# Kernel tuning notes

Measured on AMD Instinct MI355X. Metric: run time of the kernel, lower is better.

Reference implementation:

```python
import jax, jax.numpy as jnp
import numpy as np

B, T, DIM = 4, 1024, 2048
N_HEADS, N_KV_HEADS = 32, 8
HEAD_DIM = DIM // N_HEADS  # 64
N_REPS = N_HEADS // N_KV_HEADS  # 4


def setup_inputs() -> dict:
    key = jax.random.key(0)
    ks = jax.random.split(key, 8)
    # RoPE tables: theta = 10000^{-2i/d}, positions 0..T-1
    inv_freq = 1.0 / (10000.0 ** (jnp.arange(0, HEAD_DIM, 2, dtype=jnp.float32) / HEAD_DIM))
    angles = jnp.arange(T, dtype=jnp.float32)[:, None] * inv_freq[None, :]  # (T, HEAD_DIM//2)
    s = 0.02
    return {
        "input": jax.random.normal(ks[0], (B, T, DIM), jnp.float32),
        "freqs_cos": jnp.cos(angles),
        "freqs_sin": jnp.sin(angles),
        "mask": jnp.tril(jnp.ones((T, T), dtype=bool)),  # causal boolean mask
        "wq": s * jax.random.normal(ks[1], (DIM, DIM), jnp.float32),
        "wk": s * jax.random.normal(ks[2], (N_KV_HEADS * HEAD_DIM, DIM), jnp.float32),
        "wv": s * jax.random.normal(ks[3], (N_KV_HEADS * HEAD_DIM, DIM), jnp.float32),
        "wo": s * jax.random.normal(ks[4], (DIM, DIM), jnp.float32),
        "curr_pos": 0,
    }


def _apply_rope(x, cos, sin):
    # x: (B, T, H, D); cos/sin: (T, D//2). Complex multiply on (even, odd) pairs.
    xr = x[..., 0::2]
    xi = x[..., 1::2]
    c = cos[None, :, None, :]
    s = sin[None, :, None, :]
    out_r = xr * c - xi * s
    out_i = xr * s + xi * c
    return jnp.stack([out_r, out_i], axis=-1).reshape(x.shape)


def reference(input, freqs_cos, freqs_sin, mask, wq, wk, wv, wo, curr_pos):
    Bv, Tv = input.shape[0], input.shape[1]
    qs = (input @ wq.T).reshape(Bv, Tv, N_HEADS, HEAD_DIM)
    ks = (input @ wk.T).reshape(Bv, Tv, N_KV_HEADS, HEAD_DIM)
    vs = (input @ wv.T).reshape(Bv, Tv, N_KV_HEADS, HEAD_DIM)
    qs = _apply_rope(qs, freqs_cos, freqs_sin)
    ks = _apply_rope(ks, freqs_cos, freqs_sin)

    # KV cache (prefill path: curr_pos == 0, fresh cache of length 2T)
    kv_cache = jnp.zeros((Bv, 2 * Tv, N_KV_HEADS, HEAD_DIM, 2), input.dtype)
    kv_cache = kv_cache.at[:, curr_pos:curr_pos + Tv, :, :, 0].set(ks)
    kv_cache = kv_cache.at[:, curr_pos:curr_pos + Tv, :, :, 1].set(vs)
    k_all = kv_cache[:, :curr_pos + Tv, :, :, 0]
    v_all = kv_cache[:, :curr_pos + Tv, :, :, 1]

    # GQA: broadcast each kv head across its query-head group (avoid repeat_interleave copy)
    S = k_all.shape[1]
    q = qs.transpose(0, 2, 1, 3).reshape(Bv, N_KV_HEADS, N_REPS, Tv, HEAD_DIM)
    k = k_all.transpose(0, 2, 1, 3)  # (B, KVH, S, D)
    v = v_all.transpose(0, 2, 1, 3)

    scale = 1.0 / jnp.sqrt(jnp.asarray(HEAD_DIM, input.dtype))
    scores = jnp.einsum("bgrqd,bgkd->bgrqk", q, k) * scale  # (B, KVH, REPS, T, S)
    neg = jnp.asarray(jnp.finfo(input.dtype).min, input.dtype)
    scores = jnp.where(mask[None, None, None, :, :S], scores, neg)
    attn = jax.nn.softmax(scores, axis=-1)
    out = jnp.einsum("bgrqk,bgkd->bgrqd", attn, v)
    out = out.reshape(Bv, N_HEADS, Tv, HEAD_DIM).transpose(0, 2, 1, 3).reshape(Bv, Tv, DIM)
    return out @ wo.T
```

## Files before the change

### kernel.cpp

```cpp
#include <hip/hip_runtime.h>
#include <cstdint>

typedef __bf16 bf16x8 __attribute__((ext_vector_type(8)));
typedef float  f32x4  __attribute__((ext_vector_type(4)));
typedef float  f32x16 __attribute__((ext_vector_type(16)));
typedef float  float8v __attribute__((ext_vector_type(8)));
typedef unsigned short ushort8v __attribute__((ext_vector_type(8)));
typedef unsigned short ushort4v __attribute__((ext_vector_type(4)));
typedef unsigned int   uint4v   __attribute__((ext_vector_type(4)));

__device__ __forceinline__ unsigned short f2b(float f) {
  uint32_t u = __builtin_bit_cast(uint32_t, f);
  u += 0x7FFFu + ((u >> 16) & 1u);
  return (unsigned short)(u >> 16);
}
__device__ __forceinline__ float b2f(unsigned short h) {
  uint32_t u = ((uint32_t)h) << 16;
  return __builtin_bit_cast(float, u);
}
__device__ __forceinline__ unsigned int cvtpk(float lo, float hi_) {
  unsigned int r;
  asm("v_cvt_pk_bf16_f32 %0, %1, %2" : "=v"(r) : "v"(lo), "v"(hi_));
  return r;
}

__device__ __forceinline__ void async16(const void* g, void* l) {
  __builtin_amdgcn_global_load_lds(
      (const __attribute__((address_space(1))) void*)g,
      (__attribute__((address_space(3))) void*)l, 16, 0, 0);
}

#define WAITVM(N)  __builtin_amdgcn_s_waitcnt(0x0F70 | ((N) & 15))

struct CvtArgs {
  const float* src[5];
  unsigned short* dst[5];
  long n[5];
};
__global__ void cvt5_kernel(CvtArgs a) {
  long base = (long)blockIdx.x * blockDim.x + threadIdx.x;
  long gstride = (long)gridDim.x * blockDim.x;
#pragma unroll 1
  for (int sg = 0; sg < 5; ++sg) {
    const float* s = a.src[sg];
    unsigned short* d = a.dst[sg];
    long n8 = a.n[sg] >> 3;
    for (long i = base; i < n8; i += gstride) {
      float8v f = *(const float8v*)(s + i * 8);
      ushort8v o;
#pragma unroll
      for (int j = 0; j < 8; ++j) o[j] = f2b(f[j]);
      *(ushort8v*)(d + i * 8) = o;
    }
  }
}

__global__ __launch_bounds__(512, 2)
void gemmQ192(const unsigned short* __restrict__ Ag, const unsigned short* __restrict__ Wg,
              unsigned short* __restrict__ Cp) {
  constexpr int K = 2048;
  constexpr int NF = 3;
  constexpr int ASLOT = 16384;
  constexpr int BSLOT = 24576;
  constexpr int N = 3072;

  extern __shared__ char lds_c[];

  const int tid = threadIdx.x;
  const int wave = tid >> 6, lane = tid & 63;
  const int wm = wave >> 2, wn = wave & 3;
  const int lr = lane & 15, lg = lane >> 4;

  const int flat = blockIdx.y * 16 + blockIdx.x;
  const int swz = (flat & 7) * 32 + (flat >> 3);
  const int m0 = (swz >> 4) * 256, n0 = (swz & 15) * 192;

  const int laneSw = (lr >> 1) * 128 + (((((lr & 1) << 2) | lg) ^ (lr >> 1)) << 4);
  const int aoff = wm * 8192 + laneSw;

  int bByte[NF], bR7[NF];
#pragma unroll
  for (int ni = 0; ni < NF; ++ni) {
    int row = wn * 48 + ni * 16 + lr;
    bByte[ni] = row * 128;
    bR7[ni] = row & 7;
  }

  f32x4 acc[8][NF] = {};
  bf16x8 af[4], bf[NF];

  auto stA = [&](int slot, int s) {
    char* sl = lds_c + slot * ASLOT;
    const int kc = s * 32;
#pragma unroll
    for (int j = 0; j < 2; ++j) {
      int q = (tid + 512 * j) * 16;
      int R = q >> 7, g2L = ((q >> 4) & 7) ^ (R & 7);
      int row = R * 2 + (g2L >> 2), kg = g2L & 3;
      async16(Ag + (size_t)(m0 + row) * K + kc + kg * 8, sl + q);
    }
  };
  auto stB = [&](int slot, int T) {
    char* sl = lds_c + 4 * ASLOT + slot * BSLOT;
    const int kc = T * 64;
#pragma unroll
    for (int j = 0; j < 3; ++j) {
      int q = (tid + 512 * j) * 16;
      int row = q >> 7, c = (q >> 4) & 7;
      async16(Wg + (size_t)(n0 + row) * K + kc + ((c ^ (row & 7)) * 8), sl + q);
    }
  };

#define PH(SA, SB, MH, KH, RDB, STG, VM)                                      \
  {                                                                           \
    const char* As_ = lds_c + (SA) * ASLOT;                                   \
    _Pragma("unroll") for (int mi = 0; mi < 4; ++mi)                          \
      af[mi] = *(const bf16x8*)(As_ + aoff + ((MH) * 4 + mi) * 1024);         \
    if (RDB) {                                                                \
      const char* Bs_ = lds_c + 4 * ASLOT + (SB) * BSLOT;                     \
      _Pragma("unroll") for (int ni = 0; ni < NF; ++ni)                       \
        bf[ni] = *(const bf16x8*)(Bs_ + bByte[ni] +                           \
                                  (((((KH) << 2) | lg) ^ bR7[ni]) << 4));     \
    }                                                                         \
    STG;                                                                      \
    if ((VM) >= 0) WAITVM(VM);                                                \
    __builtin_amdgcn_s_barrier();                                             \
    __builtin_amdgcn_s_setprio(1);                                            \
    _Pragma("unroll") for (int mi = 0; mi < 4; ++mi)                          \
      _Pragma("unroll") for (int ni = 0; ni < NF; ++ni)                       \
        acc[(MH) * 4 + mi][ni] = __builtin_amdgcn_mfma_f32_16x16x32_bf16(     \
            af[mi], bf[ni], acc[(MH) * 4 + mi][ni], 0, 0, 0);                 \
    __builtin_amdgcn_s_setprio(0);                                            \
    __builtin_amdgcn_s_barrier();                                             \
  }

  stB(0, 0); stA(0, 0); stA(1, 1); stB(1, 1); stA(2, 2);
  WAITVM(5);
  __builtin_amdgcn_s_barrier();

  for (int t2 = 0; t2 < 30; t2 += 2) {
    PH(0, 0, 0, 0, true,  stA(3, 2 * t2 + 3), -1);
    PH(0, 0, 1, 0, false, (void)0, -1);
    PH(1, 0, 0, 1, true,  stA(0, 2 * t2 + 4), -1);
    PH(1, 0, 1, 1, false, stB(0, t2 + 2), 5);
    PH(2, 1, 0, 0, true,  stA(1, 2 * t2 + 5), -1);
    PH(2, 1, 1, 0, false, (void)0, -1);
    PH(3, 1, 0, 1, true,  stA(2, 2 * t2 + 6), -1);
    PH(3, 1, 1, 1, false, stB(1, t2 + 3), 5);
  }
  PH(0, 0, 0, 0, true,  stA(3, 63), -1);
  PH(0, 0, 1, 0, false, (void)0, -1);
  PH(1, 0, 0, 1, true,  (void)0, -1);
  PH(1, 0, 1, 1, false, (void)0, 0);
  PH(2, 1, 0, 0, true,  (void)0, -1);
  PH(2, 1, 1, 0, false, (void)0, -1);
  PH(3, 1, 0, 1, true,  (void)0, -1);
  PH(3, 1, 1, 1, false, (void)0, -1);
#undef PH

#pragma unroll
  for (int mig = 0; mig < 8; ++mig) {
#pragma unroll
    for (int j = 0; j < 4; ++j) {
      int row = m0 + wm * 128 + mig * 16 + lg * 4 + j;
#pragma unroll
      for (int ni = 0; ni < NF; ++ni) {
        int col = n0 + wn * 48 + ni * 16 + lr;
        Cp[(size_t)row * N + col] = f2b(acc[mig][ni][j]);
      }
    }
  }
}

template<bool F32OUT, int BN, int GX, int GY>
__global__ __launch_bounds__(512, 2)
void gemm8p(const unsigned short* __restrict__ Ag, const unsigned short* __restrict__ Wg,
            void* __restrict__ Cp, int N) {
  constexpr int K = 2048;
  constexpr int BM = 256;
  constexpr int NF = BN / 64;
  constexpr int AL = 2;
  constexpr int BL = BN / 128;
  constexpr int VMS = 2 * BL + AL;
  constexpr int ASLOT = BM * 64;
  constexpr int BSLOT = BN * 64;
  constexpr int NWG = GX * GY;
  constexpr int CPX = NWG / 8;

  extern __shared__ char lds_c[];

  const int tid = threadIdx.x;
  const int wave = tid >> 6, lane = tid & 63;
  const int wm = wave >> 2, wn = wave & 3;
  const int lr = lane & 15, lg = lane >> 4;

  const int flat = blockIdx.y * GX + blockIdx.x;
  const int swz = (flat & 7) * CPX + (flat >> 3);
  const int m0 = (swz / GX) * BM, n0 = (swz % GX) * BN;

  const int laneSw = (lr >> 1) * 128 + (((((lr & 1) << 2) | lg) ^ (lr >> 1)) << 4);
  const int aoff = wm * 128 * 64 + laneSw;
  const int boff = wn * NF * 1024 + laneSw;

  f32x4 acc[8][NF] = {};
  bf16x8 af[4], bf[NF];

  auto stA = [&](int slot, int s) {
    char* sl = lds_c + slot * ASLOT;
    const int kc = s * 32;
#pragma unroll
    for (int j = 0; j < AL; ++j) {
      int q = (tid + 512 * j) * 16;
      int R = q >> 7, g2L = ((q >> 4) & 7) ^ (R & 7);
      int row = R * 2 + (g2L >> 2), kg = g2L & 3;
      async16(Ag + (size_t)(m0 + row) * K + kc + kg * 8, sl + q);
    }
  };
  auto stB = [&](int slot, int s) {
    char* sl = lds_c + 4 * ASLOT + slot * BSLOT;
    const int kc = s * 32;
#pragma unroll
    for (int j = 0; j < BL; ++j) {
      int q = (tid + 512 * j) * 16;
      int R = q >> 7, g2L = ((q >> 4) & 7) ^ (R & 7);
      int row = R * 2 + (g2L >> 2), kg = g2L & 3;
      async16(Wg + (size_t)(n0 + row) * K + kc + kg * 8, sl + q);
    }
  };

#define PH(RSLOT, MH, RDB, STG, VM)                                           \
  {                                                                           \
    const char* As_ = lds_c + (RSLOT) * ASLOT;                                \
    _Pragma("unroll") for (int mi = 0; mi < 4; ++mi)                          \
      af[mi] = *(const bf16x8*)(As_ + aoff + ((MH) * 4 + mi) * 1024);         \
    if (RDB) {                                                                \
      const char* Bs_ = lds_c + 4 * ASLOT + (RSLOT) * BSLOT;                  \
      _Pragma("unroll") for (int ni = 0; ni < NF; ++ni)                       \
        bf[ni] = *(const bf16x8*)(Bs_ + boff + ni * 1024);                    \
    }                                                                         \
    STG;                                                                      \
    if ((VM) >= 0) WAITVM(VM);                                                \
    __builtin_amdgcn_s_barrier();                                             \
    __builtin_amdgcn_s_setprio(1);                                            \
    _Pragma("unroll") for (int mi = 0; mi < 4; ++mi)                          \
      _Pragma("unroll") for (int ni = 0; ni < NF; ++ni)                       \
        acc[(MH) * 4 + mi][ni] = __builtin_amdgcn_mfma_f32_16x16x32_bf16(     \
            af[mi], bf[ni], acc[(MH) * 4 + mi][ni], 0, 0, 0);                 \
    __builtin_amdgcn_s_setprio(0);                                            \
    __builtin_amdgcn_s_barrier();                                             \
  }

  stB(0, 0); stA(0, 0); stB(1, 1); stA(1, 1); stB(2, 2); stA(2, 2); stB(3, 3);
  WAITVM(VMS);
  __builtin_amdgcn_s_barrier();

  for (int T = 0; T < 30; T += 2) {
    const int p0 = 2 * T;
    PH(0, 0, true,  stA(3, p0 + 3), -1);
    PH(0, 1, false, stB(0, p0 + 4), -1);
    PH(1, 0, true,  stA(0, p0 + 4), -1);
    PH(1, 1, false, stB(1, p0 + 5), VMS);
    PH(2, 0, true,  stA(1, p0 + 5), -1);
    PH(2, 1, false, stB(2, p0 + 6), -1);
    PH(3, 0, true,  stA(2, p0 + 6), -1);
    PH(3, 1, false, stB(3, p0 + 7), VMS);
  }
  PH(0, 0, true,  stA(3, 63), -1);
  PH(0, 1, false, (void)0, -1);
  PH(1, 0, true,  (void)0, -1);
  PH(1, 1, false, (void)0, 0);
  PH(2, 0, true,  (void)0, -1);
  PH(2, 1, false, (void)0, -1);
  PH(3, 0, true,  (void)0, -1);
  PH(3, 1, false, (void)0, -1);
#undef PH

#pragma unroll
  for (int mig = 0; mig < 8; ++mig) {
#pragma unroll
    for (int j = 0; j < 4; ++j) {
      int row = m0 + wm * 128 + mig * 16 + lg * 4 + j;
#pragma unroll
      for (int ni = 0; ni < NF; ++ni) {
        int col = n0 + wn * (NF * 16) + ni * 16 + lr;
        float v = acc[mig][ni][j];
        if (F32OUT) ((float*)Cp)[(size_t)row * N + col] = v;
        else        ((unsigned short*)Cp)[(size_t)row * N + col] = f2b(v);
      }
    }
  }
}

__global__ __launch_bounds__(256)
void ropekv_kernel(unsigned short* __restrict__ qkv,
                   const float* __restrict__ cosb, const float* __restrict__ sinb,
                   unsigned short* __restrict__ vt) {
  const int tt0 = blockIdx.x * 64;
  const int kvh = blockIdx.y;
  const int b   = blockIdx.z;
  const int tid = threadIdx.x;

  {
    int r = tid >> 2, c0 = (tid & 3) * 16;
    int t = tt0 + r;
    unsigned short* kp = qkv + (size_t)(b * 1024 + t) * 3072 + 2048 + kvh * 64 + c0;
    const float* cb = cosb + t * 32 + c0 / 2;
    const float* sb = sinb + t * 32 + c0 / 2;
    ushort8v x0 = *(const ushort8v*)kp;
    ushort8v x1 = *(const ushort8v*)(kp + 8);
    float8v c = *(const float8v*)cb;
    float8v s = *(const float8v*)sb;
    ushort8v o0, o1;
#pragma unroll
    for (int j = 0; j < 4; ++j) {
      float xr = b2f(x0[2 * j]), xi = b2f(x0[2 * j + 1]);
      o0[2 * j]     = f2b(xr * c[j] - xi * s[j]);
      o0[2 * j + 1] = f2b(xr * s[j] + xi * c[j]);
    }
#pragma unroll
    for (int j = 0; j < 4; ++j) {
      float xr = b2f(x1[2 * j]), xi = b2f(x1[2 * j + 1]);
      o1[2 * j]     = f2b(xr * c[4 + j] - xi * s[4 + j]);
      o1[2 * j + 1] = f2b(xr * s[4 + j] + xi * c[4 + j]);
    }
    *(ushort8v*)kp = o0;
    *(ushort8v*)(kp + 8) = o1;
  }

  __shared__ unsigned short lT[64 * 68];
#pragma unroll
  for (int i = 0; i < 2; ++i) {
    int r = i * 32 + (tid >> 3), c = (tid & 7) * 8;
    const unsigned short* src = qkv + (size_t)(b * 1024 + tt0 + r) * 3072 + 2560 + kvh * 64 + c;
    ushort8v v = *(const ushort8v*)src;
    ushort4v a, b4;
#pragma unroll
    for (int j = 0; j < 4; ++j) { a[j] = v[j]; b4[j] = v[j + 4]; }
    *(ushort4v*)&lT[r * 68 + c]     = a;
    *(ushort4v*)&lT[r * 68 + c + 4] = b4;
  }
  __syncthreads();
#pragma unroll
  for (int i = 0; i < 2; ++i) {
    int d = tid & 63;
    int tt = i * 4 + (tid >> 6);
    ushort8v o;
#pragma unroll
    for (int j = 0; j < 8; ++j) o[j] = lT[(tt * 8 + j) * 68 + d];
    *(ushort8v*)&vt[((size_t)((b * 8 + kvh) * 64 + d)) * 1024 + tt0 + tt * 8] = o;
  }
}

__global__ __launch_bounds__(512, 4)
void attn_kernel(const unsigned short* __restrict__ qkv, const unsigned short* __restrict__ vt,
                 const float* __restrict__ cosb, const float* __restrict__ sinb,
                 unsigned short* __restrict__ ob) {
  const int flat = (blockIdx.z * 8 + blockIdx.y) * 16 + blockIdx.x;
  const int swzb = (flat & 7) * 64 + (flat >> 3);
  const int bx = swzb & 15, kvh = (swzb >> 4) & 7, b = swzb >> 7;

  const int tid = threadIdx.x, wave = tid >> 6, lane = tid & 63;
  const int l31 = lane & 31, hi = lane >> 5;
  const int wq = wave & 3, wh = wave >> 2;
  const int h = kvh * 4 + wq;

  const int qth = 31 - bx, qtl = bx;
  const int nth = qth / 4 + 1, ntl = qtl / 4 + 1;
  const int q0 = (wh ? qtl : qth) * 32;
  const int nt = wh ? ntl : nth;

  __shared__ unsigned short lK[2][128 * 64];
  __shared__ unsigned short lVt[2][64 * 128];

  bf16x8 qf[4];
  {
    int t = q0 + l31;
    const unsigned short* qp = qkv + (size_t)(b * 1024 + t) * 3072 + h * 64;
#pragma unroll
    for (int dk = 0; dk < 4; ++dk) {
      ushort8v q = *(const ushort8v*)(qp + dk * 16 + hi * 8);
      f32x4 c4 = *(const f32x4*)(cosb + t * 32 + dk * 8 + hi * 4);
      f32x4 s4 = *(const f32x4*)(sinb + t * 32 + dk * 8 + hi * 4);
      ushort8v o;
#pragma unroll
      for (int j = 0; j < 4; ++j) {
        float xr = b2f(q[2 * j]), xi = b2f(q[2 * j + 1]);
        o[2 * j]     = f2b(xr * c4[j] - xi * s4[j]);
        o[2 * j + 1] = f2b(xr * s4[j] + xi * c4[j]);
      }
      qf[dk] = __builtin_bit_cast(bf16x8, o);
    }
  }

  const unsigned short* kg = qkv + (size_t)(b * 1024) * 3072 + 2048 + kvh * 64;
  const unsigned short* vg = vt + (size_t)(b * 8 + kvh) * 64 * 1024;

  auto stage = [&](int kvb, int bi) {
    const int sr  = tid >> 3;
    const int scb = (tid & 7) * 16;
#pragma unroll
    for (int i = 0; i < 2; ++i) {
      int r = i * 64 + sr;
      int cb = scb ^ ((r & 7) << 4);
      async16(kg + (size_t)(kvb + r) * 3072 + (cb >> 1), &lK[bi][r * 64 + (scb >> 1)]);
    }
    const int rv0 = tid >> 4;
    const int scv = (tid & 15) * 16;
#pragma unroll
    for (int i = 0; i < 2; ++i) {
      int rv = i * 32 + rv0;
      int cbv = scv ^ ((rv & 15) << 4);
      async16(vg + (size_t)rv * 1024 + kvb + (cbv >> 1), &lVt[bi][rv * 128 + (scv >> 1)]);
    }
  };

  f32x16 oacc[2] = {};
  float m2 = -3e38f, l_run = 0.f;

  const float SC = 0.125f * 1.44269504f;

  auto chunk64 = [&](int cur, int ckvb, int c, bool lastT) {
    f32x16 sd[2] = {};
    __builtin_amdgcn_s_setprio(1);
#pragma unroll
    for (int s = 0; s < 2; ++s) {
      const int krow = c * 64 + s * 32 + l31;
      const char* kr = (const char*)lK[cur] + krow * 128;
      const int swz = (krow & 7) << 4;
#pragma unroll
      for (int dk = 0; dk < 4; ++dk) {
        bf16x8 kf = *(const bf16x8*)(kr + ((dk * 32 + hi * 16) ^ swz));
        sd[s] = __builtin_amdgcn_mfma_f32_32x32x16_bf16(kf, qf[dk], sd[s], 0, 0, 0);
      }
    }
    __builtin_amdgcn_s_setprio(0);

#pragma unroll
    for (int s = 0; s < 2; ++s)
#pragma unroll
      for (int r = 0; r < 16; ++r) {
        float v = sd[s][r] * SC;
        if (lastT) {
          int kvg = ckvb + s * 32 + (r & 3) + 8 * (r >> 2) + 4 * hi;
          if (kvg > q0 + l31) v = -3e38f;
        }
        sd[s][r] = v;
      }
    float pm = sd[0][0];
#pragma unroll
    for (int s = 0; s < 2; ++s)
#pragma unroll
      for (int r = 0; r < 16; ++r) pm = fmaxf(pm, sd[s][r]);
    pm = fmaxf(pm, __shfl_xor(pm, 32));
    if (!__all(pm <= m2 + 11.0f)) {
      float mnew = fmaxf(m2, pm);
      float alpha = exp2f(m2 - mnew);
      m2 = mnew;
      l_run *= alpha;
#pragma unroll
      for (int db = 0; db < 2; ++db)
#pragma unroll
        for (int r = 0; r < 16; ++r) oacc[db][r] *= alpha;
    }
    float tsum = 0.f;
#pragma unroll
    for (int s = 0; s < 2; ++s)
#pragma unroll
      for (int r = 0; r < 16; ++r) { float p = exp2f(sd[s][r] - m2); sd[s][r] = p; tsum += p; }
    tsum += __shfl_xor(tsum, 32);
    l_run += tsum;

    bf16x8 pf[2][2];
#pragma unroll
    for (int s = 0; s < 2; ++s)
#pragma unroll
      for (int kc = 0; kc < 2; ++kc) {
        unsigned int cA = cvtpk(sd[s][8 * kc + 0], sd[s][8 * kc + 1]);
        unsigned int cB = cvtpk(sd[s][8 * kc + 4], sd[s][8 * kc + 5]);
        unsigned int cC = cvtpk(sd[s][8 * kc + 2], sd[s][8 * kc + 3]);
        unsigned int cD = cvtpk(sd[s][8 * kc + 6], sd[s][8 * kc + 7]);
        unsigned int xA = __shfl_xor(cA, 32), xB = __shfl_xor(cB, 32);
        unsigned int xC = __shfl_xor(cC, 32), xD = __shfl_xor(cD, 32);
        uint4v u;
        u[0] = hi ? xB : cA;
        u[1] = hi ? xD : cC;
        u[2] = hi ? cB : xA;
        u[3] = hi ? cD : xC;
        pf[s][kc] = __builtin_bit_cast(bf16x8, u);
      }

    __builtin_amdgcn_s_setprio(1);
#pragma unroll
    for (int db = 0; db < 2; ++db) {
      const int row = db * 32 + l31;
      const char* vr = (const char*)lVt[cur] + row * 256;
      const int vswz = (row & 15) << 4;
#pragma unroll
      for (int s = 0; s < 2; ++s)
#pragma unroll
        for (int kc = 0; kc < 2; ++kc) {
          bf16x8 vf = *(const bf16x8*)(vr + ((c * 128 + s * 64 + kc * 32 + hi * 16) ^ vswz));
          oacc[db] = __builtin_amdgcn_mfma_f32_32x32x16_bf16(vf, pf[s][kc], oacc[db], 0, 0, 0);
        }
    }
    __builtin_amdgcn_s_setprio(0);
  };

  stage(0, 0);
  __syncthreads();

  for (int j = 0; j < nth; ++j) {
    const int cur = j & 1;
    if (j + 1 < nth) stage((j + 1) * 128, cur ^ 1);
    const int kvb = j * 128;

    if (j < nt) {
      const bool lastT = (j == nt - 1);
#pragma unroll 1
      for (int c = 0; c < 2; ++c) {
        if (kvb + c * 64 > q0 + 31) continue;
        chunk64(cur, kvb + c * 64, c, lastT);
      }
    }
    __syncthreads();
  }

  {
    float inv = 1.0f / l_run;
    unsigned short* orow = ob + (size_t)(b * 1024 + q0 + l31) * 2048 + h * 64;
#pragma unroll
    for (int db = 0; db < 2; ++db)
#pragma unroll
      for (int g = 0; g < 4; ++g) {
        int d0 = db * 32 + 8 * g + 4 * hi;
        ushort4v o;
#pragma unroll
        for (int j = 0; j < 4; ++j) o[j] = f2b(oacc[db][4 * g + j] * inv);
        *(ushort4v*)(orow + d0) = o;
      }
  }
}

extern "C" void kernel_launch(void* const* d_in, const int* in_sizes, int n_in,
                              void* d_out, int out_size, void* d_ws, size_t ws_size,
                              hipStream_t stream) {
  const float* input = (const float*)d_in[0];
  const float* fcos  = (const float*)d_in[1];
  const float* fsin  = (const float*)d_in[2];
  const float* wq = (const float*)d_in[4];
  const float* wk = (const float*)d_in[5];
  const float* wv = (const float*)d_in[6];
  const float* wo = (const float*)d_in[7];
  float* out = (float*)d_out;

  unsigned short* xb   = (unsigned short*)d_ws;
  unsigned short* wqkv = xb + (size_t)4096 * 2048;
  unsigned short* wob  = wqkv + (size_t)3072 * 2048;
  unsigned short* qkv  = wob + (size_t)2048 * 2048;
  unsigned short* ob   = qkv + (size_t)4096 * 3072;
  unsigned short* vtb  = xb;

  hipFuncSetAttribute((const void*)&gemmQ192,
                      hipFuncAttributeMaxDynamicSharedMemorySize, 114688);
  hipFuncSetAttribute((const void*)&gemm8p<true, 128, 16, 16>,
                      hipFuncAttributeMaxDynamicSharedMemorySize, 98304);

  CvtArgs ca;
  ca.src[0] = input; ca.dst[0] = xb;                        ca.n[0] = (long)4096 * 2048;
  ca.src[1] = wq;    ca.dst[1] = wqkv;                      ca.n[1] = (long)2048 * 2048;
  ca.src[2] = wk;    ca.dst[2] = wqkv + (size_t)2048 * 2048; ca.n[2] = (long)512 * 2048;
  ca.src[3] = wv;    ca.dst[3] = wqkv + (size_t)2560 * 2048; ca.n[3] = (long)512 * 2048;
  ca.src[4] = wo;    ca.dst[4] = wob;                       ca.n[4] = (long)2048 * 2048;
  hipLaunchKernelGGL(cvt5_kernel, dim3(2048), dim3(256), 0, stream, ca);

  hipLaunchKernelGGL(gemmQ192, dim3(16, 16), dim3(512), 114688,
                     stream, xb, wqkv, qkv);

  hipLaunchKernelGGL(ropekv_kernel, dim3(16, 8, 4), dim3(256), 0, stream,
                     qkv, fcos, fsin, vtb);

  hipLaunchKernelGGL(attn_kernel, dim3(16, 8, 4), dim3(512), 0, stream,
                     qkv, vtb, fcos, fsin, ob);

  hipLaunchKernelGGL((gemm8p<true, 128, 16, 16>), dim3(16, 16), dim3(512), 98304,
                     stream, ob, wob, (void*)out, 2048);
}
```

Measured before the change: 163.5 us.

## Shrink attention KV tile to 64 rows and fold softmax scale into Q

```diff
diff --git a/kernel.cpp b/kernel.cpp
--- a/kernel.cpp
+++ b/kernel.cpp
@@ -365,13 +365,14 @@
   const int h = kvh * 4 + wq;
 
   const int qth = 31 - bx, qtl = bx;
-  const int nth = qth / 4 + 1, ntl = qtl / 4 + 1;
+  const int nth = qth / 2 + 1, ntl = qtl / 2 + 1;
   const int q0 = (wh ? qtl : qth) * 32;
   const int nt = wh ? ntl : nth;
 
-  __shared__ unsigned short lK[2][128 * 64];
-  __shared__ unsigned short lVt[2][64 * 128];
-
+  __shared__ unsigned short lK[2][64 * 64];
+  __shared__ unsigned short lVt[2][64 * 64];
+
+  const float SC = 0.125f * 1.44269504f;
   bf16x8 qf[4];
   {
     int t = q0 + l31;
@@ -385,8 +386,8 @@
 #pragma unroll
       for (int j = 0; j < 4; ++j) {
         float xr = b2f(q[2 * j]), xi = b2f(q[2 * j + 1]);
-        o[2 * j]     = f2b(xr * c4[j] - xi * s4[j]);
-        o[2 * j + 1] = f2b(xr * s4[j] + xi * c4[j]);
+        o[2 * j]     = f2b((xr * c4[j] - xi * s4[j]) * SC);
+        o[2 * j + 1] = f2b((xr * s4[j] + xi * c4[j]) * SC);
       }
       qf[dk] = __builtin_bit_cast(bf16x8, o);
     }
@@ -398,33 +399,25 @@
   auto stage = [&](int kvb, int bi) {
     const int sr  = tid >> 3;
     const int scb = (tid & 7) * 16;
-#pragma unroll
-    for (int i = 0; i < 2; ++i) {
-      int r = i * 64 + sr;
-      int cb = scb ^ ((r & 7) << 4);
-      async16(kg + (size_t)(kvb + r) * 3072 + (cb >> 1), &lK[bi][r * 64 + (scb >> 1)]);
-    }
-    const int rv0 = tid >> 4;
-    const int scv = (tid & 15) * 16;
-#pragma unroll
-    for (int i = 0; i < 2; ++i) {
-      int rv = i * 32 + rv0;
-      int cbv = scv ^ ((rv & 15) << 4);
-      async16(vg + (size_t)rv * 1024 + kvb + (cbv >> 1), &lVt[bi][rv * 128 + (scv >> 1)]);
+    {
+      int cb = scb ^ ((sr & 7) << 4);
+      async16(kg + (size_t)(kvb + sr) * 3072 + (cb >> 1), &lK[bi][sr * 64 + (scb >> 1)]);
+    }
+    {
+      int cbv = scb ^ ((sr & 7) << 4);
+      async16(vg + (size_t)sr * 1024 + kvb + (cbv >> 1), &lVt[bi][sr * 64 + (scb >> 1)]);
     }
   };
 
   f32x16 oacc[2] = {};
   float m2 = -3e38f, l_run = 0.f;
 
-  const float SC = 0.125f * 1.44269504f;
-
-  auto chunk64 = [&](int cur, int ckvb, int c, bool lastT) {
+  auto chunk64 = [&](int cur, int ckvb, bool lastT) {
     f32x16 sd[2] = {};
     __builtin_amdgcn_s_setprio(1);
 #pragma unroll
     for (int s = 0; s < 2; ++s) {
-      const int krow = c * 64 + s * 32 + l31;
+      const int krow = s * 32 + l31;
       const char* kr = (const char*)lK[cur] + krow * 128;
       const int swz = (krow & 7) << 4;
 #pragma unroll
@@ -435,17 +428,15 @@
     }
     __builtin_amdgcn_s_setprio(0);
 
-#pragma unroll
-    for (int s = 0; s < 2; ++s)
-#pragma unroll
-      for (int r = 0; r < 16; ++r) {
-        float v = sd[s][r] * SC;
-        if (lastT) {
+    if (lastT) {
+#pragma unroll
+      for (int s = 0; s < 2; ++s)
+#pragma unroll
+        for (int r = 0; r < 16; ++r) {
           int kvg = ckvb + s * 32 + (r & 3) + 8 * (r >> 2) + 4 * hi;
-          if (kvg > q0 + l31) v = -3e38f;
+          if (kvg > q0 + l31) sd[s][r] = -3e38f;
         }
-        sd[s][r] = v;
-      }
+    }
     float pm = sd[0][0];
 #pragma unroll
     for (int s = 0; s < 2; ++s)
@@ -493,13 +484,13 @@
 #pragma unroll
     for (int db = 0; db < 2; ++db) {
       const int row = db * 32 + l31;
-      const char* vr = (const char*)lVt[cur] + row * 256;
-      const int vswz = (row & 15) << 4;
+      const char* vr = (const char*)lVt[cur] + row * 128;
+      const int vswz = (row & 7) << 4;
 #pragma unroll
       for (int s = 0; s < 2; ++s)
 #pragma unroll
         for (int kc = 0; kc < 2; ++kc) {
-          bf16x8 vf = *(const bf16x8*)(vr + ((c * 128 + s * 64 + kc * 32 + hi * 16) ^ vswz));
+          bf16x8 vf = *(const bf16x8*)(vr + ((s * 64 + kc * 32 + hi * 16) ^ vswz));
           oacc[db] = __builtin_amdgcn_mfma_f32_32x32x16_bf16(vf, pf[s][kc], oacc[db], 0, 0, 0);
         }
     }
@@ -511,17 +502,8 @@
 
   for (int j = 0; j < nth; ++j) {
     const int cur = j & 1;
-    if (j + 1 < nth) stage((j + 1) * 128, cur ^ 1);
-    const int kvb = j * 128;
-
-    if (j < nt) {
-      const bool lastT = (j == nt - 1);
-#pragma unroll 1
-      for (int c = 0; c < 2; ++c) {
-        if (kvb + c * 64 > q0 + 31) continue;
-        chunk64(cur, kvb + c * 64, c, lastT);
-      }
-    }
+    if (j + 1 < nth) stage((j + 1) * 64, cur ^ 1);
+    if (j < nt) chunk64(cur, j * 64, j == nt - 1);
     __syncthreads();
   }
 
```

After: 157.0 us. -4.0%, faster.
